# Optimization experiments

Measured on AMD Instinct MI355X. Metric: run time of the kernel, lower is better.

## Reference

```python
import math
import jax, jax.numpy as jnp
import numpy as np

HEAD_DIM = 128
N_HEADS = 64    # n_local_heads
N_KV = 8        # n_local_kv_heads
N_REP = 8       # GQA group size


def setup_inputs() -> dict:
    key = jax.random.key(0)
    ks = jax.random.split(key, 6)
    bsz, seqlen, d = 32, 1, 8192
    start_pos = 4095
    T = start_pos + seqlen  # 4096 total KV length
    x = jax.random.normal(ks[0], (bsz, seqlen, d), jnp.float32)
    wqkv_w = jax.random.normal(ks[1], (8192, 10240), jnp.float32) * 0.02  # used as x @ W
    wo_w = jax.random.normal(ks[2], (8192, 8192), jnp.float32) * 0.02    # torch Linear weight (out,in)
    theta = jax.random.uniform(ks[3], (seqlen, HEAD_DIM // 2), jnp.float32) * (2.0 * np.pi)
    freqs_cos = jnp.cos(theta)
    freqs_sin = jnp.sin(theta)
    cache_k = jax.random.normal(ks[4], (bsz, T, N_KV, HEAD_DIM), jnp.float32)
    cache_v = jax.random.normal(ks[5], (bsz, T, N_KV, HEAD_DIM), jnp.float32)
    mask = jnp.zeros((1, 1, 1, T), jnp.float32)
    return {"x": x, "cache_k": cache_k, "cache_v": cache_v, "wqkv_w": wqkv_w,
            "wo_w": wo_w, "freqs_cos": freqs_cos, "freqs_sin": freqs_sin,
            "mask": mask, "start_pos": start_pos}


def _rope(t, cos, sin):
    # t: [b, s, h, d]; cos/sin: [s, d//2]. Complex mult on interleaved (re, im) pairs.
    tr = t.reshape(*t.shape[:-1], -1, 2)
    c = cos[None, :, None, :]
    s = sin[None, :, None, :]
    re = tr[..., 0] * c - tr[..., 1] * s
    im = tr[..., 0] * s + tr[..., 1] * c
    return jnp.stack([re, im], axis=-1).reshape(t.shape)


def reference(x, cache_k, cache_v, wqkv_w, wo_w, freqs_cos, freqs_sin, mask, start_pos):
    bsz, seqlen, _ = x.shape
    blk_q = N_REP * HEAD_DIM  # 1024
    blk = blk_q + HEAD_DIM + HEAD_DIM  # 1280: interleaved q|k|v block
    # fused qkv projection, then split interleaved blocks
    xqkv = jnp.einsum('bsd,dn->bsn', x, wqkv_w).reshape(bsz, seqlen, -1, blk)
    xq = xqkv[..., :blk_q].reshape(bsz, seqlen, N_HEADS, HEAD_DIM)
    xk = xqkv[..., blk_q:blk_q + HEAD_DIM].reshape(bsz, seqlen, N_KV, HEAD_DIM)
    xv = xqkv[..., blk_q + HEAD_DIM:].reshape(bsz, seqlen, N_KV, HEAD_DIM)
    # rotary embedding on q and k
    xq = _rope(xq, freqs_cos, freqs_sin)
    xk = _rope(xk, freqs_cos, freqs_sin)
    # KV-cache write
    cache_k = jax.lax.dynamic_update_slice(cache_k, xk, (0, start_pos, 0, 0))
    cache_v = jax.lax.dynamic_update_slice(cache_v, xv, (0, start_pos, 0, 0))
    T = start_pos + seqlen
    keys = cache_k[:, :T]     # [b, T, kv, d]
    values = cache_v[:, :T]
    # GQA: group q-heads by kv-head instead of materializing repeat_kv (same math)
    q = xq.transpose(0, 2, 1, 3).reshape(bsz, N_KV, N_REP, seqlen, HEAD_DIM)
    scores = jnp.einsum('bkrsd,btkd->bkrst', q, keys) / math.sqrt(HEAD_DIM)
    scores = scores + mask  # mask [1,1,1,T] broadcasts over (r, s, t)
    probs = jax.nn.softmax(scores, axis=-1)
    out = jnp.einsum('bkrst,btkd->bkrsd', probs, values)
    out = out.reshape(bsz, N_HEADS, seqlen, HEAD_DIM).transpose(0, 2, 1, 3).reshape(bsz, seqlen, -1)
    return out @ wo_w.T
```

## Files before the change

### kernel.cpp

```cpp
#include <hip/hip_runtime.h>
#include <hip/hip_bf16.h>
#include <math.h>

typedef float  f32x4 __attribute__((ext_vector_type(4)));
typedef short  s16x8 __attribute__((ext_vector_type(8)));

#define B_   32
#define D_   8192
#define NQ   10240
#define T_   4096
#define NKV  8
#define HD   128
#define BLKW 1280
#define KSPLIT 16
#define KC   512

__device__ inline short f2bf(float f) {
  union { float f; unsigned u; } v; v.f = f;
  unsigned r = (v.u + 0x7FFFu + ((v.u >> 16) & 1u)) >> 16;
  return (short)r;
}

__device__ inline s16x8 pack8(float4 a, float4 b) {
  s16x8 r;
  r[0]=f2bf(a.x); r[1]=f2bf(a.y); r[2]=f2bf(a.z); r[3]=f2bf(a.w);
  r[4]=f2bf(b.x); r[5]=f2bf(b.y); r[6]=f2bf(b.z); r[7]=f2bf(b.w);
  return r;
}

__global__ __launch_bounds__(256) void k_qkv(const float* __restrict__ x,
                                             const float* __restrict__ W,
                                             float* __restrict__ p1) {
  int tid  = threadIdx.x;
  int lane = tid & 63, wv = tid >> 6;
  int l15  = lane & 15, lg = lane >> 4;
  int n0   = blockIdx.x * 128 + wv * 32;
  int k0   = blockIdx.y * KC;

  f32x4 acc00 = (f32x4)0.f, acc01 = (f32x4)0.f;
  f32x4 acc10 = (f32x4)0.f, acc11 = (f32x4)0.f;

  const float* xr0 = x + (size_t)l15 * D_ + k0 + lg * 8;
  const float* xr1 = x + (size_t)(16 + l15) * D_ + k0 + lg * 8;
  const float* wc0 = W + (size_t)k0 * NQ + n0 + l15;

  #pragma unroll 2
  for (int ks = 0; ks < KC; ks += 32) {
    float4 a0a = *(const float4*)(xr0 + ks);
    float4 a0b = *(const float4*)(xr0 + ks + 4);
    float4 a1a = *(const float4*)(xr1 + ks);
    float4 a1b = *(const float4*)(xr1 + ks + 4);
    const float* wk = wc0 + (size_t)(ks + lg * 8) * NQ;
    float w0[8], w1[8];
    #pragma unroll
    for (int j = 0; j < 8; ++j) {
      w0[j] = wk[(size_t)j * NQ];
      w1[j] = wk[(size_t)j * NQ + 16];
    }
    s16x8 af0 = pack8(a0a, a0b);
    s16x8 af1 = pack8(a1a, a1b);
    s16x8 bf0, bf1;
    #pragma unroll
    for (int j = 0; j < 8; ++j) { bf0[j] = f2bf(w0[j]); bf1[j] = f2bf(w1[j]); }
    acc00 = __builtin_amdgcn_mfma_f32_16x16x32_bf16(af0, bf0, acc00, 0, 0, 0);
    acc01 = __builtin_amdgcn_mfma_f32_16x16x32_bf16(af0, bf1, acc01, 0, 0, 0);
    acc10 = __builtin_amdgcn_mfma_f32_16x16x32_bf16(af1, bf0, acc10, 0, 0, 0);
    acc11 = __builtin_amdgcn_mfma_f32_16x16x32_bf16(af1, bf1, acc11, 0, 0, 0);
  }

  size_t base = (size_t)(blockIdx.y * 32) * NQ;
  #pragma unroll
  for (int r = 0; r < 4; ++r) {
    p1[base + (size_t)(lg * 4 + r) * NQ + n0 + l15]           = acc00[r];
    p1[base + (size_t)(lg * 4 + r) * NQ + n0 + 16 + l15]      = acc01[r];
    p1[base + (size_t)(16 + lg * 4 + r) * NQ + n0 + l15]      = acc10[r];
    p1[base + (size_t)(16 + lg * 4 + r) * NQ + n0 + 16 + l15] = acc11[r];
  }
}

__global__ void k_reduce_rope(const float* __restrict__ p1,
                              const float* __restrict__ fcos, const float* __restrict__ fsin,
                              float* __restrict__ qs, float* __restrict__ knew,
                              float* __restrict__ vnew) {
  int b = blockIdx.y;
  int j = (blockIdx.x * 256 + threadIdx.x) * 2;
  float v0 = 0.f, v1 = 0.f;
  #pragma unroll
  for (int c = 0; c < KSPLIT; ++c) {
    const float2 p = *(const float2*)(p1 + (size_t)(c * 32 + b) * NQ + j);
    v0 += p.x; v1 += p.y;
  }
  int g = j / BLKW;
  int r = j - g * BLKW;
  if (r < 1024) {
    int h = r >> 7, d = r & 127, dp = d >> 1;
    float c = fcos[dp], s = fsin[dp];
    const float sc = 0.08838834764831845f;
    float* q = qs + ((size_t)(b * NKV + g) * 8 + h) * HD + d;
    q[0] = (v0 * c - v1 * s) * sc;
    q[1] = (v0 * s + v1 * c) * sc;
  } else if (r < 1152) {
    int d = r - 1024, dp = d >> 1;
    float c = fcos[dp], s = fsin[dp];
    float* kp = knew + (size_t)(b * NKV + g) * HD + d;
    kp[0] = v0 * c - v1 * s;
    kp[1] = v0 * s + v1 * c;
  } else {
    int d = r - 1152;
    float* vp = vnew + (size_t)(b * NKV + g) * HD + d;
    vp[0] = v0; vp[1] = v1;
  }
}

__global__ __launch_bounds__(256) void k_attn(const float* __restrict__ cK,
                                              const float* __restrict__ cV,
                                              const float* __restrict__ qs,
                                              const float* __restrict__ knew,
                                              const float* __restrict__ vnew,
                                              float* __restrict__ pml,
                                              float* __restrict__ pacc) {
  __shared__ __align__(16) short Plds[4][2][16][32];
  int bid  = blockIdx.x;
  int pair = bid >> 2, tc = bid & 3;
  int b = pair >> 3, kv = pair & 7;
  int tid = threadIdx.x;
  int w = tid >> 6, lane = tid & 63;
  int l15 = lane & 15, lg = lane >> 4;

  for (int idx = lane; idx < 512; idx += 64) {
    int buf = idx >> 8, rem = idx & 255;
    Plds[w][buf][8 + (rem >> 5)][rem & 31] = 0;
  }

  s16x8 aq[4];
  const float* qrow = qs + ((size_t)(b * NKV + kv) * 8 + l15) * HD;
  #pragma unroll
  for (int dt = 0; dt < 4; ++dt) {
    if (l15 < 8) {
      float4 fa = *(const float4*)(qrow + dt * 32 + lg * 8);
      float4 fb = *(const float4*)(qrow + dt * 32 + lg * 8 + 4);
      aq[dt] = pack8(fa, fb);
    } else {
      s16x8 z = {0,0,0,0,0,0,0,0};
      aq[dt] = z;
    }
  }

  float m[4], lsum[4];
  #pragma unroll
  for (int r = 0; r < 4; ++r) { m[r] = -INFINITY; lsum[r] = 0.f; }
  f32x4 acc[8];
  #pragma unroll
  for (int dt = 0; dt < 8; ++dt) acc[dt] = (f32x4)0.f;

  const size_t bkv_off = (size_t)b * T_ * NKV * HD + (size_t)kv * HD;
  const float* knp = knew + (size_t)(b * NKV + kv) * HD;
  const float* vnp = vnew + (size_t)(b * NKV + kv) * HD;

  for (int tile = 0; tile < 8; ++tile) {
    int t0 = tc * 1024 + (w * 8 + tile) * 32;
    int pb = tile & 1;

    f32x4 s0 = (f32x4)0.f, s1 = (f32x4)0.f;
    {
      int trow = t0 + l15;
      const float* krow = (trow == 4095) ? knp : (cK + bkv_off + (size_t)trow * (NKV * HD));
      #pragma unroll
      for (int dt = 0; dt < 4; ++dt) {
        float4 fa = *(const float4*)(krow + dt * 32 + lg * 8);
        float4 fb = *(const float4*)(krow + dt * 32 + lg * 8 + 4);
        s16x8 bk = pack8(fa, fb);
        s0 = __builtin_amdgcn_mfma_f32_16x16x32_bf16(aq[dt], bk, s0, 0, 0, 0);
      }
    }
    {
      int trow = t0 + 16 + l15;
      const float* krow = (trow == 4095) ? knp : (cK + bkv_off + (size_t)trow * (NKV * HD));
      #pragma unroll
      for (int dt = 0; dt < 4; ++dt) {
        float4 fa = *(const float4*)(krow + dt * 32 + lg * 8);
        float4 fb = *(const float4*)(krow + dt * 32 + lg * 8 + 4);
        s16x8 bk = pack8(fa, fb);
        s1 = __builtin_amdgcn_mfma_f32_16x16x32_bf16(aq[dt], bk, s1, 0, 0, 0);
      }
    }

    float p0[4], p1v[4], scale[4];
    #pragma unroll
    for (int r = 0; r < 4; ++r) {
      float tm = fmaxf(s0[r], s1[r]);
      #pragma unroll
      for (int off = 1; off < 16; off <<= 1) tm = fmaxf(tm, __shfl_xor(tm, off));
      float mn = fmaxf(m[r], tm);
      scale[r] = __expf(m[r] - mn);
      p0[r]  = __expf(s0[r] - mn);
      p1v[r] = __expf(s1[r] - mn);
      float rsum = p0[r] + p1v[r];
      #pragma unroll
      for (int off = 1; off < 16; off <<= 1) rsum += __shfl_xor(rsum, off);
      lsum[r] = lsum[r] * scale[r] + rsum;
      m[r] = mn;
    }
    #pragma unroll
    for (int dt = 0; dt < 8; ++dt) {
      #pragma unroll
      for (int r = 0; r < 4; ++r) acc[dt][r] *= scale[r];
    }

    if (lg < 2) {
      #pragma unroll
      for (int r = 0; r < 4; ++r) {
        int h = lg * 4 + r;
        Plds[w][pb][h][l15]      = f2bf(p0[r]);
        Plds[w][pb][h][16 + l15] = f2bf(p1v[r]);
      }
    }
    asm volatile("s_waitcnt lgkmcnt(0)" ::: "memory");
    s16x8 ap = *(const s16x8*)&Plds[w][pb][l15][lg * 8];

    const float* vrow[8];
    #pragma unroll
    for (int jj = 0; jj < 8; ++jj) {
      int tr = t0 + lg * 8 + jj;
      vrow[jj] = (tr == 4095) ? vnp : (cV + bkv_off + (size_t)tr * (NKV * HD));
    }
    #pragma unroll
    for (int dt = 0; dt < 8; ++dt) {
      s16x8 bv;
      #pragma unroll
      for (int jj = 0; jj < 8; ++jj) bv[jj] = f2bf(vrow[jj][dt * 16 + l15]);
      acc[dt] = __builtin_amdgcn_mfma_f32_16x16x32_bf16(ap, bv, acc[dt], 0, 0, 0);
    }
  }

  int widx = bid * 4 + w;
  if (lg < 2) {
    #pragma unroll
    for (int r = 0; r < 4; ++r) {
      int h = lg * 4 + r;
      if (l15 == 0) {
        pml[widx * 16 + h]     = m[r];
        pml[widx * 16 + 8 + h] = lsum[r];
      }
      #pragma unroll
      for (int dt = 0; dt < 8; ++dt)
        pacc[(size_t)widx * 1024 + h * 128 + dt * 16 + l15] = acc[dt][r];
    }
  }
}

__global__ void k_attn_combine(const float* __restrict__ pml,
                               const float* __restrict__ pacc,
                               float* __restrict__ o) {
  int pair = blockIdx.x;
  int tid = threadIdx.x;
  #pragma unroll
  for (int cc = 0; cc < 4; ++cc) {
    int cell = cc * 256 + tid;
    int h = cell >> 7;
    float mstar = -INFINITY;
    #pragma unroll
    for (int w2 = 0; w2 < 16; ++w2)
      mstar = fmaxf(mstar, pml[(pair * 16 + w2) * 16 + h]);
    float L = 0.f, val = 0.f;
    #pragma unroll
    for (int w2 = 0; w2 < 16; ++w2) {
      float mw = pml[(pair * 16 + w2) * 16 + h];
      float lw = pml[(pair * 16 + w2) * 16 + 8 + h];
      float f = __expf(mw - mstar);
      L += lw * f;
      val += f * pacc[(size_t)(pair * 16 + w2) * 1024 + cell];
    }
    o[(size_t)pair * 1024 + cell] = val / L;
  }
}

__global__ __launch_bounds__(256) void k_oproj(const float* __restrict__ o,
                                               const float* __restrict__ wo,
                                               float* __restrict__ p2) {
  int tid = threadIdx.x;
  int w = tid >> 6, lane = tid & 63, l15 = lane & 15, lg = lane >> 4;
  int i0 = blockIdx.x * 64 + w * 16;
  int jc = blockIdx.y * 1024;
  f32x4 acc0 = (f32x4)0.f, acc1 = (f32x4)0.f;
  const float* orow0 = o + (size_t)l15 * D_;
  const float* orow1 = o + (size_t)(16 + l15) * D_;
  const float* wrow  = wo + (size_t)(i0 + l15) * D_;
  for (int j = jc; j < jc + 1024; j += 32) {
    int off = j + lg * 8;
    float4 a0 = *(const float4*)(orow0 + off), a0b = *(const float4*)(orow0 + off + 4);
    float4 a1 = *(const float4*)(orow1 + off), a1b = *(const float4*)(orow1 + off + 4);
    float4 b0 = *(const float4*)(wrow + off),  b0b = *(const float4*)(wrow + off + 4);
    s16x8 fa0 = pack8(a0, a0b);
    s16x8 fa1 = pack8(a1, a1b);
    s16x8 fb  = pack8(b0, b0b);
    acc0 = __builtin_amdgcn_mfma_f32_16x16x32_bf16(fa0, fb, acc0, 0, 0, 0);
    acc1 = __builtin_amdgcn_mfma_f32_16x16x32_bf16(fa1, fb, acc1, 0, 0, 0);
  }
  size_t base = (size_t)blockIdx.y * (B_ * D_);
  #pragma unroll
  for (int r = 0; r < 4; ++r) {
    p2[base + (size_t)(lg * 4 + r) * D_ + i0 + l15]      = acc0[r];
    p2[base + (size_t)(16 + lg * 4 + r) * D_ + i0 + l15] = acc1[r];
  }
}

__global__ void k_final(const float* __restrict__ p2, float* __restrict__ out) {
  int g = blockIdx.x * 256 + threadIdx.x;
  float s = 0.f;
  #pragma unroll
  for (int c = 0; c < 8; ++c) s += p2[(size_t)c * (B_ * D_) + g];
  out[g] = s;
}

extern "C" void kernel_launch(void* const* d_in, const int* in_sizes, int n_in,
                              void* d_out, int out_size, void* d_ws, size_t ws_size,
                              hipStream_t stream) {
  const float* x    = (const float*)d_in[0];
  const float* cK   = (const float*)d_in[1];
  const float* cV   = (const float*)d_in[2];
  const float* wqkv = (const float*)d_in[3];
  const float* wo   = (const float*)d_in[4];
  const float* fcos = (const float*)d_in[5];
  const float* fsin = (const float*)d_in[6];

  float* W = (float*)d_ws;
  float* qs     = W + 262144;
  float* knew   = W + 524288;
  float* vnew   = W + 557056;
  float* o      = W + 589824;
  float* shared = W + 851968;
  float* p1   = shared;
  float* pml  = shared;
  float* pacc = shared + 65536;
  float* p2   = shared;
  float* outF = (float*)d_out;

  k_qkv<<<dim3(80, KSPLIT), 256, 0, stream>>>(x, wqkv, p1);
  k_reduce_rope<<<dim3(20, 32), 256, 0, stream>>>(p1, fcos, fsin, qs, knew, vnew);
  k_attn<<<1024, 256, 0, stream>>>(cK, cV, qs, knew, vnew, pml, pacc);
  k_attn_combine<<<256, 256, 0, stream>>>(pml, pacc, o);
  k_oproj<<<dim3(128, 8), 256, 0, stream>>>(o, wo, p2);
  k_final<<<1024, 256, 0, stream>>>(p2, outF);
}
```

Before: 438.6 us.

## Double-buffer W tiles into LDS via async global_load_lds in QKV GEMM

The QKV projection kernel now stages each 32x128 tile of W into shared memory with direct global-to-LDS loads, double-buffered so the next tile's fetch overlaps the current MFMA work. Previously each lane issued strided scalar loads straight from global memory. The aim is more coalesced 16-byte loads and hidden memory latency on this bandwidth-bound weight stream. In exchange it adds 32 KB of LDS per block and a barrier every iteration, which may cut occupancy.

```diff
diff --git a/kernel.cpp b/kernel.cpp
--- a/kernel.cpp
+++ b/kernel.cpp
@@ -4,6 +4,7 @@
 
 typedef float  f32x4 __attribute__((ext_vector_type(4)));
 typedef short  s16x8 __attribute__((ext_vector_type(8)));
+typedef unsigned int u32;
 
 #define B_   32
 #define D_   8192
@@ -31,10 +32,12 @@
 __global__ __launch_bounds__(256) void k_qkv(const float* __restrict__ x,
                                              const float* __restrict__ W,
                                              float* __restrict__ p1) {
+  __shared__ float wtile[2][32 * 128];
   int tid  = threadIdx.x;
   int lane = tid & 63, wv = tid >> 6;
   int l15  = lane & 15, lg = lane >> 4;
-  int n0   = blockIdx.x * 128 + wv * 32;
+  int nblk = blockIdx.x * 128;
+  int n0   = nblk + wv * 32;
   int k0   = blockIdx.y * KC;
 
   f32x4 acc00 = (f32x4)0.f, acc01 = (f32x4)0.f;
@@ -42,31 +45,54 @@
 
   const float* xr0 = x + (size_t)l15 * D_ + k0 + lg * 8;
   const float* xr1 = x + (size_t)(16 + l15) * D_ + k0 + lg * 8;
-  const float* wc0 = W + (size_t)k0 * NQ + n0 + l15;
-
-  #pragma unroll 2
+
+  #define STAGE(buf, ks)                                                        \
+    {                                                                           \
+      const float* src = W + (size_t)(k0 + (ks)) * NQ + nblk;                   \
+      _Pragma("unroll")                                                         \
+      for (int i = 0; i < 4; ++i) {                                             \
+        int p = i * 256 + tid;                                                  \
+        const float* gp = src + (size_t)(p >> 5) * NQ + (p & 31) * 4;           \
+        __builtin_amdgcn_global_load_lds(                                       \
+            (const __attribute__((address_space(1))) u32*)gp,                   \
+            (__attribute__((address_space(3))) u32*)&wtile[buf][p * 4],         \
+            16, 0, 0);                                                          \
+      }                                                                         \
+    }
+
+  STAGE(0, 0);
+  __syncthreads();
+
+  int buf = 0;
   for (int ks = 0; ks < KC; ks += 32) {
+    if (ks + 32 < KC) STAGE(buf ^ 1, ks + 32);
+
     float4 a0a = *(const float4*)(xr0 + ks);
     float4 a0b = *(const float4*)(xr0 + ks + 4);
     float4 a1a = *(const float4*)(xr1 + ks);
     float4 a1b = *(const float4*)(xr1 + ks + 4);
-    const float* wk = wc0 + (size_t)(ks + lg * 8) * NQ;
-    float w0[8], w1[8];
-    #pragma unroll
-    for (int j = 0; j < 8; ++j) {
-      w0[j] = wk[(size_t)j * NQ];
-      w1[j] = wk[(size_t)j * NQ + 16];
-    }
     s16x8 af0 = pack8(a0a, a0b);
     s16x8 af1 = pack8(a1a, a1b);
+
+    const float* wt = &wtile[buf][wv * 32 + l15];
     s16x8 bf0, bf1;
     #pragma unroll
-    for (int j = 0; j < 8; ++j) { bf0[j] = f2bf(w0[j]); bf1[j] = f2bf(w1[j]); }
+    for (int j = 0; j < 8; ++j) {
+      float w0 = wt[(lg * 8 + j) * 128];
+      float w1 = wt[(lg * 8 + j) * 128 + 16];
+      bf0[j] = f2bf(w0);
+      bf1[j] = f2bf(w1);
+    }
+
     acc00 = __builtin_amdgcn_mfma_f32_16x16x32_bf16(af0, bf0, acc00, 0, 0, 0);
     acc01 = __builtin_amdgcn_mfma_f32_16x16x32_bf16(af0, bf1, acc01, 0, 0, 0);
     acc10 = __builtin_amdgcn_mfma_f32_16x16x32_bf16(af1, bf0, acc10, 0, 0, 0);
     acc11 = __builtin_amdgcn_mfma_f32_16x16x32_bf16(af1, bf1, acc11, 0, 0, 0);
-  }
+
+    __syncthreads();
+    buf ^= 1;
+  }
+  #undef STAGE
 
   size_t base = (size_t)(blockIdx.y * 32) * NQ;
   #pragma unroll
```

Result: no change. 445.6 us (+1.6%).
